# Optimization experiments

Measured on AMD Instinct MI355X. Metric: run time of the kernel, lower is better.

Reference implementation:

```python
import jax, jax.numpy as jnp
import numpy as np

# Dimensions matching init_kwargs
B, T, F = 256, 512, 128
COH_PTS, BULK_PTS, OUT_LEN = 64, 128, 6
COH_SIZE = 2 * COH_PTS            # fc11 out
IN_BULK = F + COH_PTS             # fc12 in
BULK_SIZE = 3 * BULK_PTS          # fc12 out

# Material constants (Turon cohesive bilinear law + J2 plasticity w/ linear hardening)
DELTA0, DELTAF = 0.01, 0.1        # damage onset / final equivalent jump
E_MOD, NU = 1.0e3, 0.3
G_MOD = E_MOD / (2.0 * (1.0 + NU))
SIG_Y, HARD = 10.0, 100.0
EPS = 1e-12
LEAKY_SLOPE = 0.01


def _plane_stress_D():
    c = E_MOD / (1.0 - NU * NU)
    return jnp.array([[c, c * NU, 0.0],
                      [c * NU, c, 0.0],
                      [0.0, 0.0, c * (1.0 - NU) / 2.0]], dtype=jnp.float32)


def setup_inputs() -> dict:
    key = jax.random.key(0)
    k_x, k_w11, k_b11, k_w12, k_w2 = jax.random.split(key, 5)
    scale11 = 1.0 / np.sqrt(F)
    scale12 = 1.0 / np.sqrt(IN_BULK)
    scale2 = 1.0 / np.sqrt(BULK_SIZE)
    return {
        "x": jax.random.normal(k_x, (B, T, F), dtype=jnp.float32),
        "W11": jax.random.normal(k_w11, (COH_SIZE, F), dtype=jnp.float32) * scale11,
        "b11": jax.random.normal(k_b11, (COH_SIZE,), dtype=jnp.float32) * scale11,
        "W12": jax.random.normal(k_w12, (BULK_SIZE, IN_BULK), dtype=jnp.float32) * scale12,
        "W2": jax.random.normal(k_w2, (OUT_LEN, BULK_SIZE), dtype=jnp.float32) * scale2,
    }


def reference(x, W11, b11, W12, W2):
    b, t, f = x.shape
    coh_pts = W11.shape[0] // 2
    bulk_pts = W12.shape[0] // 3
    D = _plane_stress_D()

    # fc11 (leaky-relu linear) is history-free -> vectorize over all timesteps
    jumps = jax.nn.leaky_relu(jnp.einsum('btf,cf->btc', x, W11) + b11,
                              LEAKY_SLOPE).reshape(b, t, coh_pts, 2)

    def step(carry, inp):
        dmg, ep = carry                      # [b, coh_pts], [b, bulk_pts]
        x_t, jump_t = inp                    # [b, f], [b, coh_pts, 2]

        # --- Turon cohesive update: monotone bilinear damage on equivalent jump ---
        jn = jax.nn.relu(jump_t[..., 0])     # tension-only normal jump
        js = jump_t[..., 1]
        delta = jnp.sqrt(jn * jn + js * js + EPS)
        d_new = jnp.clip(DELTAF * (delta - DELTA0)
                         / (jnp.maximum(delta, EPS) * (DELTAF - DELTA0)), 0.0, 1.0)
        dmg = jnp.maximum(dmg, d_new)        # commit: damage never heals

        # --- midini = cat(input, damages) -> fc12 (no bias) ---
        midini = jnp.concatenate([x_t, dmg], axis=-1)          # [b, f+coh_pts]
        strain = (midini @ W12.T).reshape(b, bulk_pts, 3)       # [b, bulk_pts, 3]

        # --- J2 plasticity (plane stress, radial return, linear hardening) ---
        sig_tr = jnp.einsum('bpi,ji->bpj', strain, D)           # trial stress
        sxx, syy, txy = sig_tr[..., 0], sig_tr[..., 1], sig_tr[..., 2]
        seq = jnp.sqrt(sxx * sxx - sxx * syy + syy * syy + 3.0 * txy * txy + EPS)
        fyield = seq - (SIG_Y + HARD * ep)
        dep = jnp.where(fyield > 0.0, fyield / (3.0 * G_MOD + HARD), 0.0)
        ep = ep + dep                                           # commit history
        scale = jnp.where(fyield > 0.0, (SIG_Y + HARD * ep) / seq, 1.0)
        sig = sig_tr * scale[..., None]

        # --- fc2 (softLayer: linear no bias + softplus) ---
        out_t = jax.nn.softplus(sig.reshape(b, -1) @ W2.T)      # [b, out_len]
        return (dmg, ep), out_t

    carry0 = (jnp.zeros((b, coh_pts), jnp.float32),
              jnp.zeros((b, bulk_pts), jnp.float32))
    _, out = jax.lax.scan(step, carry0,
                          (jnp.swapaxes(x, 0, 1), jnp.swapaxes(jumps, 0, 1)))
    return jnp.swapaxes(out, 0, 1)           # [b, t, out_len]
```

## Files before the change

### kernel.cpp

```cpp
#include <hip/hip_runtime.h>
#include <hip/hip_bf16.h>
#include <math.h>

#define NB 256
#define NT 512
#define NF 128
#define NCOH 64
#define NIN 192
#define NBS 384
#define NROWS (NB*NT)

#define C11 1098.9010989010989f
#define C12 329.67032967032966f
#define C33 384.61538461538464f
#define H3G 1253.8461538461538f
#define HOVER 0.07975460122699386f

typedef __attribute__((ext_vector_type(8))) short bf16x8;
typedef __attribute__((ext_vector_type(4))) float f32x4;
typedef __attribute__((ext_vector_type(8))) unsigned short ushort8v;
typedef __attribute__((ext_vector_type(4))) unsigned short ushort4v;

#define WAITCNT_VM(N) __builtin_amdgcn_s_waitcnt(0x0F70 | ((N) & 15) | (((N) >> 4) << 14))

#define PS ((size_t)NROWS * 32)
__device__ unsigned short g_Ahi[6 * PS];
__device__ unsigned short g_Bres[2 * NBS * NIN];
__device__ unsigned short g_W11res[32768];

static __device__ __forceinline__ unsigned short f2bf(float v) {
    __hip_bfloat16 h = __float2bfloat16(v);
    return *reinterpret_cast<unsigned short*>(&h);
}
static __device__ __forceinline__ float bf2f(unsigned short u) {
    unsigned int x = ((unsigned int)u) << 16;
    return *reinterpret_cast<float*>(&x);
}
static __device__ __forceinline__ void async_copy16(const void* g, void* l) {
    __builtin_amdgcn_global_load_lds(
        (const __attribute__((address_space(1))) unsigned int*)g,
        (__attribute__((address_space(3))) unsigned int*)l, 16, 0, 0);
}

__global__ __launch_bounds__(256) void k0_w12(const float* __restrict__ W12)
{
    const int idx = blockIdx.x * 256 + threadIdx.x;
    const int e    = idx & 7;
    const int l    = (idx >> 3) & 63;
    const int nf   = (idx >> 9) & 3;
    const int part = (idx >> 11) & 1;
    const int kc   = (idx >> 12) % 6;
    const int nblk = idx / 24576;
    const int n = nblk * 64 + nf * 16 + (l & 15);
    const int k = kc * 32 + (l >> 4) * 8 + e;
    const int p = n / 3, j = n - 3 * p;
    const float* w = W12 + (size_t)(3 * p) * NIN;
    float v;
    if (j == 0)      v = C11 * w[k]           + C12 * w[NIN + k];
    else if (j == 1) v = C12 * w[k]           + C11 * w[NIN + k];
    else             v = C33 * w[2 * NIN + k];
    unsigned short h = f2bf(v);
    g_Bres[idx] = part ? f2bf(v - bf2f(h)) : h;
}

__global__ __launch_bounds__(256) void k0b_w11(const float* __restrict__ W11)
{
    const int idx = blockIdx.x * 256 + threadIdx.x;
    const int e    = idx & 7;
    const int l    = (idx >> 3) & 63;
    const int nf   = (idx >> 9) & 7;
    const int part = (idx >> 12) & 1;
    const int kc   = idx >> 13;
    const int n = nf * 16 + (l & 15);
    const int k = kc * 32 + (l >> 4) * 8 + e;
    const float v = W11[(size_t)n * NF + k];
    unsigned short h = f2bf(v);
    g_W11res[idx] = part ? f2bf(v - bf2f(h)) : h;
}

__global__ __launch_bounds__(256) void k1_fc11(
    const float* __restrict__ x, const float* __restrict__ b11,
    unsigned short* __restrict__ dnT)
{
    __shared__ unsigned short Ws[32768];

    const int tid = threadIdx.x;
    const int lane = tid & 63, w = tid >> 6;
    const int fr = lane & 15, fq = lane >> 4;
    const int xbase = blockIdx.x * 128 + w * 32;

#pragma unroll
    for (int i = 0; i < 16; ++i)
        async_copy16((const char*)g_W11res + tid * 16 + i * 4096,
                     (char*)Ws + tid * 16 + i * 4096);

    f32x4 acc[8][2];
#pragma unroll
    for (int q = 0; q < 8; ++q)
#pragma unroll
        for (int f = 0; f < 2; ++f) acc[q][f] = (f32x4){0.f, 0.f, 0.f, 0.f};

    WAITCNT_VM(0);
    __builtin_amdgcn_s_barrier();

#pragma unroll
    for (int kc = 0; kc < 4; ++kc) {
        bf16x8 ah[2], al[2];
#pragma unroll
        for (int f = 0; f < 2; ++f) {
            const int row = xbase + f * 16 + fr;
            const float* xs = x + (size_t)row * NF + kc * 32 + fq * 8;
            float4 v0 = ((const float4*)xs)[0];
            float4 v1 = ((const float4*)xs)[1];
            float v[8] = {v0.x, v0.y, v0.z, v0.w, v1.x, v1.y, v1.z, v1.w};
            ushort8v h, lo;
#pragma unroll
            for (int i = 0; i < 8; ++i) {
                h[i]  = f2bf(v[i]);
                lo[i] = f2bf(v[i] - bf2f(h[i]));
            }
            *(ushort8v*)(g_Ahi + (size_t)kc * PS + (size_t)row * 32 + fq * 8) = h;
            ah[f] = *reinterpret_cast<bf16x8*>(&h);
            al[f] = *reinterpret_cast<bf16x8*>(&lo);
        }
#pragma unroll
        for (int q = 0; q < 8; ++q) {
            bf16x8 wh = *(const bf16x8*)&Ws[(kc * 16 + q) * 512 + lane * 8];
            bf16x8 wl = *(const bf16x8*)&Ws[(kc * 16 + 8 + q) * 512 + lane * 8];
#pragma unroll
            for (int f = 0; f < 2; ++f) {
                acc[q][f] = __builtin_amdgcn_mfma_f32_16x16x32_bf16(
                    wh, ah[f], acc[q][f], 0, 0, 0);
                acc[q][f] = __builtin_amdgcn_mfma_f32_16x16x32_bf16(
                    wl, ah[f], acc[q][f], 0, 0, 0);
                acc[q][f] = __builtin_amdgcn_mfma_f32_16x16x32_bf16(
                    wh, al[f], acc[q][f], 0, 0, 0);
            }
        }
    }

#pragma unroll
    for (int q = 0; q < 8; ++q) {
        float4 bv = *(const float4*)(b11 + q * 16 + fq * 4);
#pragma unroll
        for (int f = 0; f < 2; ++f) {
            const int xrow = xbase + f * 16 + fr;
            float z[4] = {acc[q][f][0] + bv.x, acc[q][f][1] + bv.y,
                          acc[q][f][2] + bv.z, acc[q][f][3] + bv.w};
#pragma unroll
            for (int pr = 0; pr < 2; ++pr) {
                float jn = fmaxf(z[2 * pr], 0.0f);
                float zs = z[2 * pr + 1];
                float js = (zs > 0.0f) ? zs : 0.01f * zs;
                float delta = sqrtf(jn * jn + js * js + 1e-12f);
                float dn = 0.1f * (delta - 0.01f) / (fmaxf(delta, 1e-12f) * 0.09f);
                dn = fminf(fmaxf(dn, 0.0f), 1.0f);
                dnT[(size_t)(q * 8 + fq * 2 + pr) * NROWS + xrow] = f2bf(dn);
            }
        }
    }
}

__global__ __launch_bounds__(64) void k2a(const unsigned short* __restrict__ dnT,
                                          float* __restrict__ totals)
{
    const int b = blockIdx.x >> 3, seg = blockIdx.x & 7;
    const int c = threadIdx.x;
    const ushort8v* p = (const ushort8v*)(dnT + (size_t)c * NROWS + b * NT + seg * 64);
    float m = 0.0f;
#pragma unroll
    for (int g = 0; g < 8; ++g) {
        ushort8v v = p[g];
#pragma unroll
        for (int i = 0; i < 8; ++i) m = fmaxf(m, bf2f(v[i]));
    }
    totals[(size_t)(b * 8 + seg) * 64 + c] = m;
}

__global__ __launch_bounds__(64) void k2b(const unsigned short* __restrict__ dnT,
                                          const float* __restrict__ totals)
{
    const int b = blockIdx.x >> 3, seg = blockIdx.x & 7;
    const int c = threadIdx.x;
    float carry = 0.0f;
    for (int s = 0; s < seg; ++s)
        carry = fmaxf(carry, totals[(size_t)(b * 8 + s) * 64 + c]);
    const ushort8v* p = (const ushort8v*)(dnT + (size_t)c * NROWS + b * NT + seg * 64);
    unsigned short* ah = g_Ahi + (size_t)(4 + (c >> 5)) * PS
                       + (size_t)(b * NT + seg * 64) * 32 + (c & 31);
    float m = carry;
#pragma unroll
    for (int g = 0; g < 8; ++g) {
        ushort8v v = p[g];
#pragma unroll
        for (int i = 0; i < 8; ++i) {
            m = fmaxf(m, bf2f(v[i]));
            ah[(size_t)(g * 8 + i) * 32] = f2bf(m);
        }
    }
}

__global__ __launch_bounds__(256, 3) void k3_mfma(unsigned short* __restrict__ sigT)
{
    __shared__ unsigned short Bs[24576];

    const int tid = threadIdx.x;
    const int lane = tid & 63, w = tid >> 6;
    const int id = blockIdx.x;
    const int sw = (id & 7) * 384 + (id >> 3);
    const int nblk = sw % 6;
    const int m0 = (sw / 6) * 256;
    const int n0 = nblk * 64;
    const int wm = w * 64;
    const int fr = lane & 15, fq = lane >> 4;

    const size_t abase = (size_t)(m0 + wm + fr) * 32 + fq * 8;

    bf16x8 a0[4], a1[4];
#pragma unroll
    for (int mi = 0; mi < 4; ++mi)
        a0[mi] = *(const bf16x8*)(g_Ahi + abase + mi * 512);

    {
        const char* bsrc = (const char*)g_Bres + (size_t)nblk * 49152;
#pragma unroll
        for (int i = 0; i < 12; ++i)
            async_copy16(bsrc + tid * 16 + i * 4096, (char*)Bs + tid * 16 + i * 4096);
    }
    WAITCNT_VM(0);
    __builtin_amdgcn_s_barrier();

    f32x4 acc[4][4];
#pragma unroll
    for (int mi = 0; mi < 4; ++mi)
#pragma unroll
        for (int ni = 0; ni < 4; ++ni) acc[mi][ni] = (f32x4){0.f, 0.f, 0.f, 0.f};

#pragma unroll
    for (int c = 0; c < 6; ++c) {
        bf16x8* acur = (c & 1) ? a1 : a0;
        bf16x8* anxt = (c & 1) ? a0 : a1;
        if (c < 5) {
#pragma unroll
            for (int mi = 0; mi < 4; ++mi)
                anxt[mi] = *(const bf16x8*)(g_Ahi + (size_t)(c + 1) * PS
                                            + abase + mi * 512);
        }
        bf16x8 bh[4], bl[4];
#pragma unroll
        for (int ni = 0; ni < 4; ++ni) {
            bh[ni] = *(const bf16x8*)&Bs[((c * 8 + ni) << 9) + lane * 8];
            bl[ni] = *(const bf16x8*)&Bs[((c * 8 + 4 + ni) << 9) + lane * 8];
        }
#pragma unroll
        for (int mi = 0; mi < 4; ++mi)
#pragma unroll
            for (int ni = 0; ni < 4; ++ni) {
                acc[mi][ni] = __builtin_amdgcn_mfma_f32_16x16x32_bf16(
                    acur[mi], bh[ni], acc[mi][ni], 0, 0, 0);
                acc[mi][ni] = __builtin_amdgcn_mfma_f32_16x16x32_bf16(
                    acur[mi], bl[ni], acc[mi][ni], 0, 0, 0);
            }
    }

    __syncthreads();
    unsigned short* T = Bs;
#pragma unroll
    for (int mi = 0; mi < 4; ++mi)
#pragma unroll
        for (int ni = 0; ni < 4; ++ni) {
            const int cIdx = ni * 16 + fr;
            const int tloc = wm + mi * 16 + fq * 4;
            ushort4v h;
#pragma unroll
            for (int r = 0; r < 4; ++r) h[r] = f2bf(acc[mi][ni][r]);
            *(ushort4v*)&T[cIdx * 272 + tloc] = h;
        }
    __syncthreads();

    const int b_idx = m0 >> 9;
    const int tq = lane & 31, c2 = lane >> 5;
    const size_t colbase = (((size_t)(b_idx * NBS + n0)) << 9) + (m0 & 511);
#pragma unroll
    for (int it = 0; it < 8; ++it) {
        const int cc = w * 16 + it * 2 + c2;
        ushort8v v = *(const ushort8v*)&T[cc * 272 + tq * 8];
        *(ushort8v*)(sigT + colbase + ((size_t)cc << 9) + tq * 8) = v;
    }
}

#define PFD 8
__global__ __launch_bounds__(128) void k4_scan(
    const unsigned short* __restrict__ sigT, unsigned short* __restrict__ uT)
{
    const int b = blockIdx.x;
    const int p = threadIdx.x;
    const ushort8v* sx = (const ushort8v*)(sigT + (((size_t)(b * NBS + 3 * p    )) << 9));
    const ushort8v* sy = (const ushort8v*)(sigT + (((size_t)(b * NBS + 3 * p + 1)) << 9));
    const ushort8v* sz = (const ushort8v*)(sigT + (((size_t)(b * NBS + 3 * p + 2)) << 9));
    ushort8v* uo = (ushort8v*)(uT + (((size_t)(b * 128 + p)) << 9));

    ushort8v px[PFD], py[PFD], pz[PFD];
#pragma unroll
    for (int g = 0; g < PFD; ++g) { px[g] = sx[g]; py[g] = sy[g]; pz[g] = sz[g]; }

    float u = 10.0f;
#pragma unroll 8
    for (int g = 0; g < 64 - PFD; ++g) {
        const int sl = g & (PFD - 1);
        ushort8v vx = px[sl], vy = py[sl], vz = pz[sl];
        px[sl] = sx[g + PFD]; py[sl] = sy[g + PFD]; pz[sl] = sz[g + PFD];
        ushort8v ov;
#pragma unroll
        for (int i = 0; i < 8; ++i) {
            float sxx = bf2f(vx[i]), syy = bf2f(vy[i]), txy = bf2f(vz[i]);
            float e = sxx*sxx - sxx*syy + syy*syy + 3.0f*txy*txy + 1e-12f;
            float seq = sqrtf(e);
            u = fmaf(fmaxf(seq - u, 0.0f), HOVER, u);
            ov[i] = f2bf(u);
        }
        uo[g] = ov;
    }
#pragma unroll
    for (int g = 64 - PFD; g < 64; ++g) {
        const int sl = g & (PFD - 1);
        ushort8v vx = px[sl], vy = py[sl], vz = pz[sl];
        ushort8v ov;
#pragma unroll
        for (int i = 0; i < 8; ++i) {
            float sxx = bf2f(vx[i]), syy = bf2f(vy[i]), txy = bf2f(vz[i]);
            float e = sxx*sxx - sxx*syy + syy*syy + 3.0f*txy*txy + 1e-12f;
            float seq = sqrtf(e);
            u = fmaf(fmaxf(seq - u, 0.0f), HOVER, u);
            ov[i] = f2bf(u);
        }
        uo[g] = ov;
    }
}

__global__ __launch_bounds__(256) void k5_out(
    const unsigned short* __restrict__ sigT, const unsigned short* __restrict__ uT,
    const float* __restrict__ W2, float* __restrict__ out)
{
    __shared__ float W2s[6][NBS];
    const int tid = threadIdx.x;
    for (int i = tid; i < 6 * NBS; i += 256) W2s[i / NBS][i % NBS] = W2[i];
    __syncthreads();

    const int b = blockIdx.x >> 1;
    const int t = (blockIdx.x & 1) * 256 + tid;
    const unsigned short* sb = sigT + (((size_t)b * NBS) << 9) + t;
    const unsigned short* ub = uT + (((size_t)b * 128) << 9) + t;

    float acc[6] = {0, 0, 0, 0, 0, 0};
#pragma unroll 4
    for (int p = 0; p < 128; ++p) {
        float sxx = bf2f(sb[(size_t)(3 * p    ) << 9]);
        float syy = bf2f(sb[(size_t)(3 * p + 1) << 9]);
        float txy = bf2f(sb[(size_t)(3 * p + 2) << 9]);
        float u   = bf2f(ub[(size_t)p << 9]);
        float e = sxx*sxx - sxx*syy + syy*syy + 3.0f*txy*txy + 1e-12f;
        float scale = fminf(1.0f, u * rsqrtf(e));
        float fx = sxx * scale, fy = syy * scale, fz = txy * scale;
#pragma unroll
        for (int o = 0; o < 6; ++o) {
            acc[o] = fmaf(fx, W2s[o][3 * p    ], acc[o]);
            acc[o] = fmaf(fy, W2s[o][3 * p + 1], acc[o]);
            acc[o] = fmaf(fz, W2s[o][3 * p + 2], acc[o]);
        }
    }

    float* op = out + ((size_t)(b * NT + t)) * 6;
#pragma unroll
    for (int o = 0; o < 6; ++o) {
        float z = acc[o];
        op[o] = fmaxf(z, 0.0f) + log1pf(expf(-fabsf(z)));
    }
}

extern "C" void kernel_launch(void* const* d_in, const int* in_sizes, int n_in,
                              void* d_out, int out_size, void* d_ws, size_t ws_size,
                              hipStream_t stream)
{
    const float* x   = (const float*)d_in[0];
    const float* W11 = (const float*)d_in[1];
    const float* b11 = (const float*)d_in[2];
    const float* W12 = (const float*)d_in[3];
    const float* W2  = (const float*)d_in[4];
    float* out = (float*)d_out;

    unsigned short* dnT = (unsigned short*)d_ws;
    unsigned short* uT = (unsigned short*)d_ws;
    unsigned short* sigT = (unsigned short*)((char*)d_ws + (size_t)NROWS * NCOH * sizeof(float));
    float* totals = (float*)((char*)d_ws + (size_t)128 * 1024 * 1024);

    k0_w12<<<(2 * NBS * NIN) / 256, 256, 0, stream>>>(W12);
    k0b_w11<<<128, 256, 0, stream>>>(W11);
    k1_fc11<<<NROWS / 128, 256, 0, stream>>>(x, b11, dnT);
    k2a<<<NB * 8, 64, 0, stream>>>(dnT, totals);
    k2b<<<NB * 8, 64, 0, stream>>>(dnT, totals);
    k3_mfma<<<3072, 256, 0, stream>>>(sigT);
    k4_scan<<<NB, 128, 0, stream>>>(sigT, uT);
    k5_out<<<NROWS / 256, 256, 0, stream>>>(sigT, uT, W2, out);
}
```

Measured before the change: 263.3 us.

## Warp-specialize scan kernel: producer waves compute seq into LDS, consumers run recurrence

The scan kernel grows from 128 to 512 threads. Six producer waves load the stress components, compute the equivalent stress and write it into a double-buffered, XOR-swizzled LDS tile. Two consumer waves run only the serial hardening recurrence on precomputed values, chunk by chunk. The aim is to take the loads and the sqrt off the serial critical path and add memory parallelism, at the cost of a barrier per chunk and 64KB of LDS per block. Producer global loads are now scalar 2-byte gathers rather than 16-byte vector loads.

Result: faster. 255.9 us (-2.8%).

```diff
diff --git a/kernel.cpp b/kernel.cpp
--- a/kernel.cpp
+++ b/kernel.cpp
@@ -289,52 +289,68 @@
     }
 }
 
-#define PFD 8
-__global__ __launch_bounds__(128) void k4_scan(
+#define K4CH 64
+__global__ __launch_bounds__(512) void k4_scan(
     const unsigned short* __restrict__ sigT, unsigned short* __restrict__ uT)
 {
+    __shared__ float Sq[2][128 * K4CH];
+
+    const int tid = threadIdx.x;
     const int b = blockIdx.x;
-    const int p = threadIdx.x;
-    const ushort8v* sx = (const ushort8v*)(sigT + (((size_t)(b * NBS + 3 * p    )) << 9));
-    const ushort8v* sy = (const ushort8v*)(sigT + (((size_t)(b * NBS + 3 * p + 1)) << 9));
-    const ushort8v* sz = (const ushort8v*)(sigT + (((size_t)(b * NBS + 3 * p + 2)) << 9));
-    ushort8v* uo = (ushort8v*)(uT + (((size_t)(b * 128 + p)) << 9));
-
-    ushort8v px[PFD], py[PFD], pz[PFD];
-#pragma unroll
-    for (int g = 0; g < PFD; ++g) { px[g] = sx[g]; py[g] = sy[g]; pz[g] = sz[g]; }
+    const int w = tid >> 6;
+
+    if (w >= 2) {
+        for (int idx = tid - 128; idx < 128 * K4CH; idx += 384) {
+            const int t = idx & (K4CH - 1);
+            const int p = idx >> 6;
+            const size_t cb = ((size_t)(b * NBS + 3 * p)) << 9;
+            float sxx = bf2f(sigT[cb + t]);
+            float syy = bf2f(sigT[cb + 512 + t]);
+            float txy = bf2f(sigT[cb + 1024 + t]);
+            float e = sxx*sxx - sxx*syy + syy*syy + 3.0f*txy*txy + 1e-12f;
+            Sq[0][p * K4CH + (t ^ (p & 31))] = sqrtf(e);
+        }
+    }
+    __syncthreads();
 
     float u = 10.0f;
-#pragma unroll 8
-    for (int g = 0; g < 64 - PFD; ++g) {
-        const int sl = g & (PFD - 1);
-        ushort8v vx = px[sl], vy = py[sl], vz = pz[sl];
-        px[sl] = sx[g + PFD]; py[sl] = sy[g + PFD]; pz[sl] = sz[g + PFD];
-        ushort8v ov;
-#pragma unroll
-        for (int i = 0; i < 8; ++i) {
-            float sxx = bf2f(vx[i]), syy = bf2f(vy[i]), txy = bf2f(vz[i]);
-            float e = sxx*sxx - sxx*syy + syy*syy + 3.0f*txy*txy + 1e-12f;
-            float seq = sqrtf(e);
-            u = fmaf(fmaxf(seq - u, 0.0f), HOVER, u);
-            ov[i] = f2bf(u);
-        }
-        uo[g] = ov;
-    }
-#pragma unroll
-    for (int g = 64 - PFD; g < 64; ++g) {
-        const int sl = g & (PFD - 1);
-        ushort8v vx = px[sl], vy = py[sl], vz = pz[sl];
-        ushort8v ov;
-#pragma unroll
-        for (int i = 0; i < 8; ++i) {
-            float sxx = bf2f(vx[i]), syy = bf2f(vy[i]), txy = bf2f(vz[i]);
-            float e = sxx*sxx - sxx*syy + syy*syy + 3.0f*txy*txy + 1e-12f;
-            float seq = sqrtf(e);
-            u = fmaf(fmaxf(seq - u, 0.0f), HOVER, u);
-            ov[i] = f2bf(u);
-        }
-        uo[g] = ov;
+    ushort8v* uo = (ushort8v*)(uT + (((size_t)(b * 128 + (tid & 127))) << 9));
+
+#pragma unroll 1
+    for (int c = 0; c < 8; ++c) {
+        if (w < 2) {
+            const int p = tid;
+            const float* S = &Sq[c & 1][p * K4CH];
+            const int pk = p & 31;
+#pragma unroll
+            for (int g = 0; g < 8; ++g) {
+                float sq[8];
+#pragma unroll
+                for (int i = 0; i < 8; ++i) sq[i] = S[(g * 8 + i) ^ pk];
+                ushort8v ov;
+#pragma unroll
+                for (int i = 0; i < 8; ++i) {
+                    u = fmaf(fmaxf(sq[i] - u, 0.0f), HOVER, u);
+                    ov[i] = f2bf(u);
+                }
+                uo[c * 8 + g] = ov;
+            }
+        } else if (c < 7) {
+            const int base = (c + 1) * K4CH;
+            float* D = Sq[(c + 1) & 1];
+            for (int idx = tid - 128; idx < 128 * K4CH; idx += 384) {
+                const int t = idx & (K4CH - 1);
+                const int p = idx >> 6;
+                const size_t cb = ((size_t)(b * NBS + 3 * p)) << 9;
+                const int tt = base + t;
+                float sxx = bf2f(sigT[cb + tt]);
+                float syy = bf2f(sigT[cb + 512 + tt]);
+                float txy = bf2f(sigT[cb + 1024 + tt]);
+                float e = sxx*sxx - sxx*syy + syy*syy + 3.0f*txy*txy + 1e-12f;
+                D[p * K4CH + (t ^ (p & 31))] = sqrtf(e);
+            }
+        }
+        __syncthreads();
     }
 }
 
@@ -400,6 +416,6 @@
     k2a<<<NB * 8, 64, 0, stream>>>(dnT, totals);
     k2b<<<NB * 8, 64, 0, stream>>>(dnT, totals);
     k3_mfma<<<3072, 256, 0, stream>>>(sigT);
-    k4_scan<<<NB, 128, 0, stream>>>(sigT, uT);
+    k4_scan<<<NB, 512, 0, stream>>>(sigT, uT);
     k5_out<<<NROWS / 256, 256, 0, stream>>>(sigT, uT, W2, out);
 }
```
